# Performance work log

Hardware: AMD Instinct MI355X
Metric: run time of the kernel (lower is better)

Reference implementation:

```python
import jax, jax.numpy as jnp
import numpy as np

B, S = 8, 2048
CHANNELS, DIM, HEADS = 256, 3, 6
TCH = CHANNELS * 2  # 512
EPS = 1e-5


def _linear_init(key, out_f, in_f):
    # torch nn.Linear default init: U(-1/sqrt(in_f), 1/sqrt(in_f)) for W and b
    k1, k2 = jax.random.split(key)
    bound = 1.0 / np.sqrt(in_f)
    w = jax.random.uniform(k1, (out_f, in_f), jnp.float32, -bound, bound)
    b = jax.random.uniform(k2, (out_f,), jnp.float32, -bound, bound)
    return w, b


def setup_inputs() -> dict:
    key = jax.random.key(0)
    ks = jax.random.split(key, 8)
    x = jax.random.normal(ks[0], (B, S, TCH), jnp.float32)
    wq, bq = _linear_init(ks[1], DIM, TCH)
    wk, bk = _linear_init(ks[2], DIM, TCH)
    wv, bv = _linear_init(ks[3], DIM, TCH)
    wo, bo = _linear_init(ks[4], TCH, HEADS * DIM)
    w1, b1 = _linear_init(ks[5], TCH, TCH)
    w2, b2 = _linear_init(ks[6], TCH, TCH)
    gamma = jnp.ones((TCH,), jnp.float32)
    beta = jnp.zeros((TCH,), jnp.float32)
    return {"x": x, "wq": wq, "bq": bq, "wk": wk, "bk": bk, "wv": wv, "bv": bv,
            "wo": wo, "bo": bo, "w1": w1, "b1": b1, "w2": w2, "b2": b2,
            "gamma": gamma, "beta": beta}


def _layernorm(x, gamma, beta):
    mu = jnp.mean(x, axis=-1, keepdims=True)
    var = jnp.mean(jnp.square(x - mu), axis=-1, keepdims=True)
    return (x - mu) * jax.lax.rsqrt(var + EPS) * gamma + beta


def reference(x, wq, bq, wk, bk, wv, bv, wo, bo, w1, b1, w2, b2, gamma, beta):
    # All heads share the same w_q/w_k/w_v, so one attention pass suffices;
    # concatenating HEADS copies reproduces the original math exactly.
    q = x @ wq.T + bq                      # [B,S,DIM]
    k = x @ wk.T + bk                      # [B,S,DIM]
    v = x @ wv.T + bv                      # [B,S,DIM]
    scores = jnp.einsum('bqd,bkd->bqk', q, k) / np.sqrt(DIM)  # [B,S,S]
    soft = jax.nn.softmax(scores, axis=-1)
    z = jnp.einsum('bqk,bkd->bqd', soft, v)  # [B,S,DIM]
    z = jnp.concatenate([z] * HEADS, axis=-1)  # [B,S,HEADS*DIM]
    z = z @ wo.T + bo                       # [B,S,TCH]
    r0 = x + (z @ w1.T + b1)
    r1 = _layernorm(r0, gamma, beta)
    r1 = r1 @ w2.T + b2
    r = r0 + r1
    return _layernorm(r, gamma, beta)
```

## Files before the change

### kernel.cpp

```cpp
#include <hip/hip_runtime.h>
#include <hip/hip_bf16.h>

#define TCH 512
#define MTOT 16384
#define SEQ 2048
#define LN_EPS 1e-5f

typedef __attribute__((ext_vector_type(8))) __bf16 bf16x8;
typedef __attribute__((ext_vector_type(4))) float f32x4;

__device__ __forceinline__ unsigned pkbf(float a, float b) {
  union { __hip_bfloat16 h; unsigned short u; } ca, cb;
  ca.h = __float2bfloat16(a); cb.h = __float2bfloat16(b);
  return (unsigned)ca.u | ((unsigned)cb.u << 16);
}
__device__ __forceinline__ float bf_lo(unsigned u) { return __uint_as_float(u << 16); }
__device__ __forceinline__ float bf_hi(unsigned u) { return __uint_as_float(u & 0xffff0000u); }

__device__ __forceinline__ bf16x8 cvt8(float4 a, float4 b) {
  union { __hip_bfloat16 h; __bf16 v; } u;
  bf16x8 r;
  u.h = __float2bfloat16(a.x); r[0] = u.v;
  u.h = __float2bfloat16(a.y); r[1] = u.v;
  u.h = __float2bfloat16(a.z); r[2] = u.v;
  u.h = __float2bfloat16(a.w); r[3] = u.v;
  u.h = __float2bfloat16(b.x); r[4] = u.v;
  u.h = __float2bfloat16(b.y); r[5] = u.v;
  u.h = __float2bfloat16(b.z); r[6] = u.v;
  u.h = __float2bfloat16(b.w); r[7] = u.v;
  return r;
}

#define QSCALE 0.8329517853860118f

__global__ __launch_bounds__(256) void prep_kernel(
    const float* __restrict__ w2,
    const float* __restrict__ wo, const float* __restrict__ bo,
    const float* __restrict__ wq, const float* __restrict__ bq,
    const float* __restrict__ wk, const float* __restrict__ bk,
    const float* __restrict__ wv, const float* __restrict__ bv,
    __hip_bfloat16* __restrict__ w2b,
    float4* __restrict__ wo_eff4,
    __hip_bfloat16* __restrict__ wqkvb, float* __restrict__ qkvbias)
{
  int i = blockIdx.x * 256 + threadIdx.x;
  w2b[i] = __float2bfloat16(w2[i]);
  if (i < TCH) {
    float s0 = 0.f, s1 = 0.f, s2 = 0.f;
    #pragma unroll
    for (int h = 0; h < 6; ++h) {
      s0 += wo[i*18 + h*3 + 0];
      s1 += wo[i*18 + h*3 + 1];
      s2 += wo[i*18 + h*3 + 2];
    }
    wo_eff4[i] = make_float4(s0, s1, s2, bo[i]);
  }
  if (i < 16 * TCH) {
    int row = i >> 9, k = i & 511;
    float v;
    if      (row < 3) v = wq[row * TCH + k] * QSCALE;
    else if (row < 6) v = wk[(row - 3) * TCH + k];
    else if (row < 9) v = wv[(row - 6) * TCH + k];
    else              v = 0.f;
    wqkvb[i] = __float2bfloat16(v);
  }
  if (i < 16) {
    float v;
    if      (i < 3) v = bq[i] * QSCALE;
    else if (i < 6) v = bk[i - 3];
    else if (i < 9) v = bv[i - 6];
    else            v = 0.f;
    qkvbias[i] = v;
  }
}

__global__ __launch_bounds__(256) void prep2_kernel(
    const float* __restrict__ w1, const float* __restrict__ b1,
    const float4* __restrict__ wo_eff4, float4* __restrict__ weff4)
{
  const int t = threadIdx.x, w = t >> 6, l = t & 63;
  const int i = blockIdx.x * 4 + w;
  float sx = 0.f, sy = 0.f, sz = 0.f, sw = 0.f;
  #pragma unroll
  for (int j = 0; j < 8; ++j) {
    const int k = j * 64 + l;
    const float a = w1[(size_t)i * TCH + k];
    const float4 e = wo_eff4[k];
    sx += a * e.x; sy += a * e.y; sz += a * e.z; sw += a * e.w;
  }
  #pragma unroll
  for (int off = 1; off < 64; off <<= 1) {
    sx += __shfl_xor(sx, off, 64);
    sy += __shfl_xor(sy, off, 64);
    sz += __shfl_xor(sz, off, 64);
    sw += __shfl_xor(sw, off, 64);
  }
  if (l == 0) weff4[i] = make_float4(sx, sy, sz, sw + b1[i]);
}

__global__ __launch_bounds__(256) void qkv_kernel(
    const float* __restrict__ x,
    const __hip_bfloat16* __restrict__ wqkvb, const float* __restrict__ qkvbias,
    float4* __restrict__ q4, uint4* __restrict__ kvp)
{
  const int t = threadIdx.x, wv = t >> 6, ln = t & 63;
  const int l16 = ln & 15, quad = ln >> 4;
  const int row0 = blockIdx.x * 16;
  const int k0 = wv * 128;

  bf16x8 bfr[4];
  #pragma unroll
  for (int ks = 0; ks < 4; ++ks)
    bfr[ks] = *reinterpret_cast<const bf16x8*>(wqkvb + l16 * TCH + k0 + ks * 32 + quad * 8);

  const float* xp = x + (size_t)(row0 + l16) * TCH + k0 + quad * 8;

  f32x4 acc = {};
  #pragma unroll
  for (int ks = 0; ks < 4; ++ks) {
    float4 a = *(const float4*)(xp + ks * 32);
    float4 b = *(const float4*)(xp + ks * 32 + 4);
    acc = __builtin_amdgcn_mfma_f32_16x16x32_bf16(cvt8(a, b), bfr[ks], acc, 0, 0, 0);
  }

  __shared__ float tr[4][16][17];
  __shared__ float fin[16][17];
  #pragma unroll
  for (int r = 0; r < 4; ++r) tr[wv][quad * 4 + r][l16] = acc[r];
  __syncthreads();

  {
    const int r = t >> 4, c = t & 15;
    fin[r][c] = tr[0][r][c] + tr[1][r][c] + tr[2][r][c] + tr[3][r][c] + qkvbias[c];
  }
  __syncthreads();

  if (t < 16) {
    q4[row0 + t] = make_float4(fin[t][0], fin[t][1], fin[t][2], 0.f);
  } else if (t < 32) {
    const int r = t - 16;
    kvp[row0 + r] = make_uint4(pkbf(fin[r][3], fin[r][4]),
                               pkbf(fin[r][5], fin[r][6]),
                               pkbf(fin[r][7], fin[r][8]), 0u);
  }
}

__global__ __launch_bounds__(1024) void attn_kernel(
    const float4* __restrict__ q4, const uint4* __restrict__ kvp,
    const float* __restrict__ x, const float4* __restrict__ weff4,
    const float* __restrict__ gamma, const float* __restrict__ beta,
    __hip_bfloat16* __restrict__ r0b, __hip_bfloat16* __restrict__ r1b)
{
  __shared__ float4 part[16 * 64];
  __shared__ float4 zbuf[64];

  const int b    = blockIdx.x >> 5;
  const int qc   = blockIdx.x & 31;
  const int base = b * SEQ;
  const int tid  = threadIdx.x;
  const int wave = tid >> 6;
  const int lane = tid & 63;
  const float4 q = q4[base + qc * 64 + lane];

  const int wu = __builtin_amdgcn_readfirstlane(wave);
  const uint4* kvw = kvp + base + wu * 128;

  float l[4] = {}, a0[4] = {}, a1[4] = {}, a2[4] = {};
  #pragma unroll 4
  for (int i = 0; i < 32; ++i) {
    #pragma unroll
    for (int s = 0; s < 4; ++s) {
      uint4 rec = kvw[s * 32 + i];
      float sc = bf_lo(rec.x) * q.x + bf_hi(rec.x) * q.y + bf_lo(rec.y) * q.z;
      float p = __builtin_amdgcn_exp2f(sc);
      l[s]  += p;
      a0[s] += p * bf_hi(rec.y);
      a1[s] += p * bf_lo(rec.z);
      a2[s] += p * bf_hi(rec.z);
    }
  }
  part[wave * 64 + lane] = make_float4(l[0]+l[1]+l[2]+l[3],
                                       a0[0]+a0[1]+a0[2]+a0[3],
                                       a1[0]+a1[1]+a1[2]+a1[3],
                                       a2[0]+a2[1]+a2[2]+a2[3]);
  __syncthreads();

  if (tid < 64) {
    float L = 0.f, A0 = 0.f, A1 = 0.f, A2 = 0.f;
    #pragma unroll
    for (int w = 0; w < 16; ++w) {
      float4 p = part[w * 64 + tid];
      L += p.x; A0 += p.y; A1 += p.z; A2 += p.w;
    }
    const float inv = 1.f / L;
    zbuf[tid] = make_float4(A0 * inv, A1 * inv, A2 * inv, 0.f);
  }
  __syncthreads();

  const int c0 = lane * 8;
  float4 wv[8];
  #pragma unroll
  for (int j = 0; j < 8; ++j) wv[j] = weff4[c0 + j];
  const float4 g0  = *(const float4*)(gamma + c0);
  const float4 g1  = *(const float4*)(gamma + c0 + 4);
  const float4 be0 = *(const float4*)(beta  + c0);
  const float4 be1 = *(const float4*)(beta  + c0 + 4);
  const float gg[8] = {g0.x,g0.y,g0.z,g0.w,g1.x,g1.y,g1.z,g1.w};
  const float bb[8] = {be0.x,be0.y,be0.z,be0.w,be1.x,be1.y,be1.z,be1.w};

  #pragma unroll
  for (int qi = 0; qi < 4; ++qi) {
    const int qloc = wave * 4 + qi;
    const int grow = base + qc * 64 + qloc;
    const float4 z = zbuf[qloc];
    const float* xr = x + (size_t)grow * TCH + c0;
    const float4 x0 = *(const float4*)xr;
    const float4 x1 = *(const float4*)(xr + 4);
    const float xv[8] = {x0.x,x0.y,x0.z,x0.w,x1.x,x1.y,x1.z,x1.w};
    float r0v[8], s = 0.f, sq = 0.f;
    #pragma unroll
    for (int j = 0; j < 8; ++j) {
      float v = xv[j] + z.x * wv[j].x + z.y * wv[j].y + z.z * wv[j].z + wv[j].w;
      r0v[j] = v; s += v; sq += v * v;
    }
    #pragma unroll
    for (int off = 1; off < 64; off <<= 1) {
      s  += __shfl_xor(s,  off, 64);
      sq += __shfl_xor(sq, off, 64);
    }
    const float mu = s * (1.f / TCH);
    const float rs = rsqrtf(sq * (1.f / TCH) - mu * mu + LN_EPS);
    *(bf16x8*)(r0b + (size_t)grow * TCH + c0) =
        cvt8(make_float4(r0v[0], r0v[1], r0v[2], r0v[3]),
             make_float4(r0v[4], r0v[5], r0v[6], r0v[7]));
    float r1v[8];
    #pragma unroll
    for (int j = 0; j < 8; ++j) r1v[j] = (r0v[j] - mu) * rs * gg[j] + bb[j];
    *(bf16x8*)(r1b + (size_t)grow * TCH + c0) =
        cvt8(make_float4(r1v[0], r1v[1], r1v[2], r1v[3]),
             make_float4(r1v[4], r1v[5], r1v[6], r1v[7]));
  }
}

__global__ __launch_bounds__(256) void gemm_kernel(
    const __hip_bfloat16* __restrict__ A,
    const __hip_bfloat16* __restrict__ W,
    const float* __restrict__ bias,
    const __hip_bfloat16* __restrict__ res,
    __hip_bfloat16* __restrict__ Cout,
    float2* __restrict__ partial)
{
  __shared__ __align__(16) __hip_bfloat16 At[2][4][128][8];
  __shared__ __align__(16) __hip_bfloat16 Wt[2][4][128][8];
  __shared__ float redS[128][2];
  __shared__ float redQ[128][2];

  const int bx   = blockIdx.x;
  const int rb   = bx & 127, cb = bx >> 7;
  const int row0 = rb * 128, col0 = cb * 128;
  const int t    = threadIdx.x;
  const int w    = t >> 6, l = t & 63;
  const int l16  = l & 15, quad = l >> 4;
  const int wr   = w >> 1, wc = w & 1;
  const int srow = t & 127;
  const int sq0  = (t >> 7) << 1;

  auto stage = [&](int ks, int b) {
    #pragma unroll
    for (int j = 0; j < 2; ++j) {
      const int q = sq0 | j;
      __builtin_amdgcn_global_load_lds(
          (const __attribute__((address_space(1))) void*)(A + (size_t)(row0 + srow) * TCH + ks * 32 + q * 8),
          (__attribute__((address_space(3))) void*)&At[b][q][srow][0], 16, 0, 0);
      __builtin_amdgcn_global_load_lds(
          (const __attribute__((address_space(1))) void*)(W + (size_t)(col0 + srow) * TCH + ks * 32 + q * 8),
          (__attribute__((address_space(3))) void*)&Wt[b][q][srow][0], 16, 0, 0);
    }
  };

  f32x4 acc[4][4] = {};
  stage(0, 0);
  for (int ks = 0; ks < 16; ++ks) {
    const int cur = ks & 1;
    __syncthreads();
    if (ks < 15) stage(ks + 1, cur ^ 1);
    bf16x8 af[4], bf[4];
    #pragma unroll
    for (int mt = 0; mt < 4; ++mt)
      af[mt] = *reinterpret_cast<const bf16x8*>(&At[cur][quad][wr * 64 + mt * 16 + l16][0]);
    #pragma unroll
    for (int nt = 0; nt < 4; ++nt)
      bf[nt] = *reinterpret_cast<const bf16x8*>(&Wt[cur][quad][wc * 64 + nt * 16 + l16][0]);
    #pragma unroll
    for (int mt = 0; mt < 4; ++mt)
      #pragma unroll
      for (int nt = 0; nt < 4; ++nt)
        acc[mt][nt] = __builtin_amdgcn_mfma_f32_16x16x32_bf16(af[mt], bf[nt], acc[mt][nt], 0, 0, 0);
  }

  #pragma unroll
  for (int mt = 0; mt < 4; ++mt) {
    #pragma unroll
    for (int r = 0; r < 4; ++r) {
      const int lrow = wr * 64 + mt * 16 + quad * 4 + r;
      const int grow = row0 + lrow;
      float s = 0.f, sq = 0.f;
      #pragma unroll
      for (int nt = 0; nt < 4; ++nt) {
        const int col = col0 + wc * 64 + nt * 16 + l16;
        float v = acc[mt][nt][r] + bias[col] + __bfloat162float(res[(size_t)grow * TCH + col]);
        Cout[(size_t)grow * TCH + col] = __float2bfloat16(v);
        s += v; sq += v * v;
      }
      #pragma unroll
      for (int off = 1; off < 16; off <<= 1) {
        s  += __shfl_xor(s,  off, 64);
        sq += __shfl_xor(sq, off, 64);
      }
      if (l16 == 0) { redS[lrow][wc] = s; redQ[lrow][wc] = sq; }
    }
  }
  __syncthreads();

  if (t < 128) {
    partial[(size_t)cb * MTOT + row0 + t] =
        make_float2(redS[t][0] + redS[t][1], redQ[t][0] + redQ[t][1]);
  }
}

template<typename OUT_T>
__global__ __launch_bounds__(256) void ln_kernel(
    const __hip_bfloat16* __restrict__ Cin, const float2* __restrict__ partial,
    const float* __restrict__ gamma, const float* __restrict__ beta,
    OUT_T* __restrict__ out)
{
  const int t = threadIdx.x, wv = t >> 6, ln = t & 63;
  const int row = blockIdx.x * 4 + wv;

  float2 p0 = partial[row];
  float2 p1 = partial[MTOT + row];
  float2 p2 = partial[2 * MTOT + row];
  float2 p3 = partial[3 * MTOT + row];
  const float S = p0.x + p1.x + p2.x + p3.x;
  const float Q = p0.y + p1.y + p2.y + p3.y;
  const float mu  = S * (1.f / TCH);
  const float var = Q * (1.f / TCH) - mu * mu;
  const float rs  = rsqrtf(var + LN_EPS);

  const int c0 = ln * 8;
  bf16x8 vr = *reinterpret_cast<const bf16x8*>(Cin + (size_t)row * TCH + c0);
  float4 g0 = *(const float4*)(gamma + c0), g1 = *(const float4*)(gamma + c0 + 4);
  float4 b0 = *(const float4*)(beta  + c0), b1 = *(const float4*)(beta  + c0 + 4);

  float o[8];
  const float gg[8] = {g0.x,g0.y,g0.z,g0.w,g1.x,g1.y,g1.z,g1.w};
  const float bb[8] = {b0.x,b0.y,b0.z,b0.w,b1.x,b1.y,b1.z,b1.w};
  #pragma unroll
  for (int j = 0; j < 8; ++j) {
    union { __bf16 v; __hip_bfloat16 h; } u; u.v = vr[j];
    o[j] = (__bfloat162float(u.h) - mu) * rs * gg[j] + bb[j];
  }

  if constexpr (sizeof(OUT_T) == 2) {
    unsigned ov[4];
    #pragma unroll
    for (int j = 0; j < 4; ++j) ov[j] = pkbf(o[2*j], o[2*j+1]);
    *(uint4*)((__hip_bfloat16*)out + (size_t)row * TCH + c0) =
        make_uint4(ov[0], ov[1], ov[2], ov[3]);
  } else {
    float* op = (float*)out + (size_t)row * TCH + c0;
    *(float4*)op       = make_float4(o[0], o[1], o[2], o[3]);
    *(float4*)(op + 4) = make_float4(o[4], o[5], o[6], o[7]);
  }
}

extern "C" void kernel_launch(void* const* d_in, const int* in_sizes, int n_in,
                              void* d_out, int out_size, void* d_ws, size_t ws_size,
                              hipStream_t stream) {
  (void)in_sizes; (void)n_in; (void)out_size; (void)ws_size;
  const float* x     = (const float*)d_in[0];
  const float* wq    = (const float*)d_in[1];
  const float* bq    = (const float*)d_in[2];
  const float* wk    = (const float*)d_in[3];
  const float* bk    = (const float*)d_in[4];
  const float* wv    = (const float*)d_in[5];
  const float* bv    = (const float*)d_in[6];
  const float* wo    = (const float*)d_in[7];
  const float* bo    = (const float*)d_in[8];
  const float* w1    = (const float*)d_in[9];
  const float* b1    = (const float*)d_in[10];
  const float* w2    = (const float*)d_in[11];
  const float* b2    = (const float*)d_in[12];
  const float* gamma = (const float*)d_in[13];
  const float* beta  = (const float*)d_in[14];
  float* out = (float*)d_out;

  char* ws = (char*)d_ws;
  size_t off = 0;
  float4* q4      = (float4*)(ws + off); off += (size_t)MTOT * 16;
  uint4*  kvp     = (uint4*)(ws + off);  off += (size_t)MTOT * 16;
  float4* wo_eff4 = (float4*)(ws + off); off += (size_t)TCH * 16;
  float4* weff4   = (float4*)(ws + off); off += (size_t)TCH * 16;
  __hip_bfloat16* w2b   = (__hip_bfloat16*)(ws + off); off += (size_t)TCH * TCH * 2;
  __hip_bfloat16* wqkvb = (__hip_bfloat16*)(ws + off); off += (size_t)16 * TCH * 2;
  float*          qkvbias = (float*)(ws + off);        off += 64;
  __hip_bfloat16* r0b = (__hip_bfloat16*)(ws + off); off += (size_t)MTOT * TCH * 2;
  __hip_bfloat16* r1b = (__hip_bfloat16*)(ws + off); off += (size_t)MTOT * TCH * 2;
  __hip_bfloat16* rrb = (__hip_bfloat16*)(ws + off); off += (size_t)MTOT * TCH * 2;
  float2* part2 = (float2*)(ws + off); off += (size_t)4 * MTOT * 8;

  prep_kernel<<<(TCH*TCH)/256, 256, 0, stream>>>(
      w2, wo, bo, wq, bq, wk, bk, wv, bv, w2b, wo_eff4, wqkvb, qkvbias);
  prep2_kernel<<<TCH/4, 256, 0, stream>>>(w1, b1, wo_eff4, weff4);
  qkv_kernel<<<MTOT/16, 256, 0, stream>>>(x, wqkvb, qkvbias, q4, kvp);
  attn_kernel<<<MTOT/64, 1024, 0, stream>>>(q4, kvp, x, weff4, gamma, beta, r0b, r1b);
  gemm_kernel<<<512, 256, 0, stream>>>(r1b, w2b, b2, r0b, rrb, part2);
  ln_kernel<float><<<MTOT/4, 256, 0, stream>>>(rrb, part2, gamma, beta, out);
}
```

Before: 178.1 us.

## Split attention into score kernel and separate residual/LayerNorm epilogue kernel

```diff
diff --git a/kernel.cpp b/kernel.cpp
--- a/kernel.cpp
+++ b/kernel.cpp
@@ -145,14 +145,12 @@
   }
 }
 
-__global__ __launch_bounds__(1024) void attn_kernel(
+__global__ __launch_bounds__(1024) void attn_score_kernel(
     const float4* __restrict__ q4, const uint4* __restrict__ kvp,
-    const float* __restrict__ x, const float4* __restrict__ weff4,
-    const float* __restrict__ gamma, const float* __restrict__ beta,
-    __hip_bfloat16* __restrict__ r0b, __hip_bfloat16* __restrict__ r1b)
-{
+    float4* __restrict__ zfin)
+{
+  __shared__ uint4  kvL[2048];
   __shared__ float4 part[16 * 64];
-  __shared__ float4 zbuf[64];
 
   const int b    = blockIdx.x >> 5;
   const int qc   = blockIdx.x & 31;
@@ -160,17 +158,19 @@
   const int tid  = threadIdx.x;
   const int wave = tid >> 6;
   const int lane = tid & 63;
+
+  kvL[tid]        = kvp[base + tid];
+  kvL[tid + 1024] = kvp[base + tid + 1024];
   const float4 q = q4[base + qc * 64 + lane];
-
-  const int wu = __builtin_amdgcn_readfirstlane(wave);
-  const uint4* kvw = kvp + base + wu * 128;
-
+  __syncthreads();
+
+  const int k0 = wave * 128;
   float l[4] = {}, a0[4] = {}, a1[4] = {}, a2[4] = {};
   #pragma unroll 4
   for (int i = 0; i < 32; ++i) {
     #pragma unroll
     for (int s = 0; s < 4; ++s) {
-      uint4 rec = kvw[s * 32 + i];
+      uint4 rec = kvL[k0 + s * 32 + i];
       float sc = bf_lo(rec.x) * q.x + bf_hi(rec.x) * q.y + bf_lo(rec.y) * q.z;
       float p = __builtin_amdgcn_exp2f(sc);
       l[s]  += p;
@@ -193,14 +193,23 @@
       L += p.x; A0 += p.y; A1 += p.z; A2 += p.w;
     }
     const float inv = 1.f / L;
-    zbuf[tid] = make_float4(A0 * inv, A1 * inv, A2 * inv, 0.f);
-  }
-  __syncthreads();
+    zfin[base + qc * 64 + tid] = make_float4(A0 * inv, A1 * inv, A2 * inv, 0.f);
+  }
+}
+
+__global__ __launch_bounds__(256) void attn_epi_kernel(
+    const float4* __restrict__ zfin, const float* __restrict__ x,
+    const float4* __restrict__ weff4,
+    const float* __restrict__ gamma, const float* __restrict__ beta,
+    __hip_bfloat16* __restrict__ r0b, __hip_bfloat16* __restrict__ r1b)
+{
+  const int t = threadIdx.x, wv = t >> 6, lane = t & 63;
+  const int row0 = blockIdx.x * 16 + wv * 4;
 
   const int c0 = lane * 8;
-  float4 wv[8];
-  #pragma unroll
-  for (int j = 0; j < 8; ++j) wv[j] = weff4[c0 + j];
+  float4 wvv[8];
+  #pragma unroll
+  for (int j = 0; j < 8; ++j) wvv[j] = weff4[c0 + j];
   const float4 g0  = *(const float4*)(gamma + c0);
   const float4 g1  = *(const float4*)(gamma + c0 + 4);
   const float4 be0 = *(const float4*)(beta  + c0);
@@ -210,9 +219,8 @@
 
   #pragma unroll
   for (int qi = 0; qi < 4; ++qi) {
-    const int qloc = wave * 4 + qi;
-    const int grow = base + qc * 64 + qloc;
-    const float4 z = zbuf[qloc];
+    const int grow = row0 + qi;
+    const float4 z = zfin[grow];
     const float* xr = x + (size_t)grow * TCH + c0;
     const float4 x0 = *(const float4*)xr;
     const float4 x1 = *(const float4*)(xr + 4);
@@ -220,7 +228,7 @@
     float r0v[8], s = 0.f, sq = 0.f;
     #pragma unroll
     for (int j = 0; j < 8; ++j) {
-      float v = xv[j] + z.x * wv[j].x + z.y * wv[j].y + z.z * wv[j].z + wv[j].w;
+      float v = xv[j] + z.x * wvv[j].x + z.y * wvv[j].y + z.z * wvv[j].z + wvv[j].w;
       r0v[j] = v; s += v; sq += v * v;
     }
     #pragma unroll
@@ -399,6 +407,7 @@
   size_t off = 0;
   float4* q4      = (float4*)(ws + off); off += (size_t)MTOT * 16;
   uint4*  kvp     = (uint4*)(ws + off);  off += (size_t)MTOT * 16;
+  float4* zfin    = (float4*)(ws + off); off += (size_t)MTOT * 16;
   float4* wo_eff4 = (float4*)(ws + off); off += (size_t)TCH * 16;
   float4* weff4   = (float4*)(ws + off); off += (size_t)TCH * 16;
   __hip_bfloat16* w2b   = (__hip_bfloat16*)(ws + off); off += (size_t)TCH * TCH * 2;
@@ -413,7 +422,8 @@
       w2, wo, bo, wq, bq, wk, bk, wv, bv, w2b, wo_eff4, wqkvb, qkvbias);
   prep2_kernel<<<TCH/4, 256, 0, stream>>>(w1, b1, wo_eff4, weff4);
   qkv_kernel<<<MTOT/16, 256, 0, stream>>>(x, wqkvb, qkvbias, q4, kvp);
-  attn_kernel<<<MTOT/64, 1024, 0, stream>>>(q4, kvp, x, weff4, gamma, beta, r0b, r1b);
+  attn_score_kernel<<<MTOT/64, 1024, 0, stream>>>(q4, kvp, zfin);
+  attn_epi_kernel<<<MTOT/16, 256, 0, stream>>>(zfin, x, weff4, gamma, beta, r0b, r1b);
   gemm_kernel<<<512, 256, 0, stream>>>(r1b, w2b, b2, r0b, rrb, part2);
   ln_kernel<float><<<MTOT/4, 256, 0, stream>>>(rrb, part2, gamma, beta, out);
 }
```

New measurement: 180.4 us. Within noise of the previous version (+1.3%).

## Fuse QKV and attention into cooperative kernel; merge weight prep kernels

Applied to the files above, without the earlier changes.

```diff
diff --git a/kernel.cpp b/kernel.cpp
--- a/kernel.cpp
+++ b/kernel.cpp
@@ -1,5 +1,8 @@
 #include <hip/hip_runtime.h>
 #include <hip/hip_bf16.h>
+#include <hip/hip_cooperative_groups.h>
+
+namespace cg = cooperative_groups;
 
 #define TCH 512
 #define MTOT 16384
@@ -39,22 +42,13 @@
     const float* __restrict__ wq, const float* __restrict__ bq,
     const float* __restrict__ wk, const float* __restrict__ bk,
     const float* __restrict__ wv, const float* __restrict__ bv,
+    const float* __restrict__ w1, const float* __restrict__ b1,
     __hip_bfloat16* __restrict__ w2b,
-    float4* __restrict__ wo_eff4,
-    __hip_bfloat16* __restrict__ wqkvb, float* __restrict__ qkvbias)
+    __hip_bfloat16* __restrict__ wqkvb, float* __restrict__ qkvbias,
+    float4* __restrict__ weff4)
 {
   int i = blockIdx.x * 256 + threadIdx.x;
   w2b[i] = __float2bfloat16(w2[i]);
-  if (i < TCH) {
-    float s0 = 0.f, s1 = 0.f, s2 = 0.f;
-    #pragma unroll
-    for (int h = 0; h < 6; ++h) {
-      s0 += wo[i*18 + h*3 + 0];
-      s1 += wo[i*18 + h*3 + 1];
-      s2 += wo[i*18 + h*3 + 2];
-    }
-    wo_eff4[i] = make_float4(s0, s1, s2, bo[i]);
-  }
   if (i < 16 * TCH) {
     int row = i >> 9, k = i & 511;
     float v;
@@ -72,80 +66,80 @@
     else            v = 0.f;
     qkvbias[i] = v;
   }
-}
-
-__global__ __launch_bounds__(256) void prep2_kernel(
-    const float* __restrict__ w1, const float* __restrict__ b1,
-    const float4* __restrict__ wo_eff4, float4* __restrict__ weff4)
-{
-  const int t = threadIdx.x, w = t >> 6, l = t & 63;
-  const int i = blockIdx.x * 4 + w;
-  float sx = 0.f, sy = 0.f, sz = 0.f, sw = 0.f;
-  #pragma unroll
-  for (int j = 0; j < 8; ++j) {
-    const int k = j * 64 + l;
-    const float a = w1[(size_t)i * TCH + k];
-    const float4 e = wo_eff4[k];
-    sx += a * e.x; sy += a * e.y; sz += a * e.z; sw += a * e.w;
-  }
-  #pragma unroll
-  for (int off = 1; off < 64; off <<= 1) {
-    sx += __shfl_xor(sx, off, 64);
-    sy += __shfl_xor(sy, off, 64);
-    sz += __shfl_xor(sz, off, 64);
-    sw += __shfl_xor(sw, off, 64);
-  }
-  if (l == 0) weff4[i] = make_float4(sx, sy, sz, sw + b1[i]);
-}
-
-__global__ __launch_bounds__(256) void qkv_kernel(
+  if (blockIdx.x < 128) {
+    const int t = threadIdx.x, w = t >> 6, l = t & 63;
+    const int row = blockIdx.x * 4 + w;
+    float sx = 0.f, sy = 0.f, sz = 0.f, sw = 0.f;
+    #pragma unroll
+    for (int j = 0; j < 8; ++j) {
+      const int k = j * 64 + l;
+      float e0 = 0.f, e1 = 0.f, e2 = 0.f;
+      #pragma unroll
+      for (int h = 0; h < 6; ++h) {
+        e0 += wo[k*18 + h*3 + 0];
+        e1 += wo[k*18 + h*3 + 1];
+        e2 += wo[k*18 + h*3 + 2];
+      }
+      const float a = w1[(size_t)row * TCH + k];
+      sx += a * e0; sy += a * e1; sz += a * e2; sw += a * bo[k];
+    }
+    #pragma unroll
+    for (int off = 1; off < 64; off <<= 1) {
+      sx += __shfl_xor(sx, off, 64);
+      sy += __shfl_xor(sy, off, 64);
+      sz += __shfl_xor(sz, off, 64);
+      sw += __shfl_xor(sw, off, 64);
+    }
+    if (l == 0) weff4[row] = make_float4(sx, sy, sz, sw + b1[row]);
+  }
+}
+
+__device__ __forceinline__ void qkv_phase(
     const float* __restrict__ x,
     const __hip_bfloat16* __restrict__ wqkvb, const float* __restrict__ qkvbias,
     float4* __restrict__ q4, uint4* __restrict__ kvp)
 {
-  const int t = threadIdx.x, wv = t >> 6, ln = t & 63;
-  const int l16 = ln & 15, quad = ln >> 4;
-  const int row0 = blockIdx.x * 16;
-  const int k0 = wv * 128;
+  __shared__ float tr[4][4][16][17];
+
+  const int tid  = threadIdx.x;
+  const int wave = tid >> 6, lane = tid & 63;
+  const int l16  = lane & 15, quad = lane >> 4;
+  const int ks4  = wave >> 2, rg = wave & 3;
+  const int grow0 = blockIdx.x * 64;
+  const int r0 = grow0 + rg * 16;
+  const int k0 = ks4 * 128;
 
   bf16x8 bfr[4];
   #pragma unroll
-  for (int ks = 0; ks < 4; ++ks)
-    bfr[ks] = *reinterpret_cast<const bf16x8*>(wqkvb + l16 * TCH + k0 + ks * 32 + quad * 8);
-
-  const float* xp = x + (size_t)(row0 + l16) * TCH + k0 + quad * 8;
-
+  for (int ksj = 0; ksj < 4; ++ksj)
+    bfr[ksj] = *reinterpret_cast<const bf16x8*>(wqkvb + l16 * TCH + k0 + ksj * 32 + quad * 8);
+
+  const float* xp = x + (size_t)(r0 + l16) * TCH + k0 + quad * 8;
   f32x4 acc = {};
   #pragma unroll
-  for (int ks = 0; ks < 4; ++ks) {
-    float4 a = *(const float4*)(xp + ks * 32);
-    float4 b = *(const float4*)(xp + ks * 32 + 4);
-    acc = __builtin_amdgcn_mfma_f32_16x16x32_bf16(cvt8(a, b), bfr[ks], acc, 0, 0, 0);
-  }
-
-  __shared__ float tr[4][16][17];
-  __shared__ float fin[16][17];
-  #pragma unroll
-  for (int r = 0; r < 4; ++r) tr[wv][quad * 4 + r][l16] = acc[r];
+  for (int ksj = 0; ksj < 4; ++ksj) {
+    float4 a = *(const float4*)(xp + ksj * 32);
+    float4 b = *(const float4*)(xp + ksj * 32 + 4);
+    acc = __builtin_amdgcn_mfma_f32_16x16x32_bf16(cvt8(a, b), bfr[ksj], acc, 0, 0, 0);
+  }
+  #pragma unroll
+  for (int r = 0; r < 4; ++r) tr[ks4][rg][quad * 4 + r][l16] = acc[r];
   __syncthreads();
 
-  {
-    const int r = t >> 4, c = t & 15;
-    fin[r][c] = tr[0][r][c] + tr[1][r][c] + tr[2][r][c] + tr[3][r][c] + qkvbias[c];
-  }
-  __syncthreads();
-
-  if (t < 16) {
-    q4[row0 + t] = make_float4(fin[t][0], fin[t][1], fin[t][2], 0.f);
-  } else if (t < 32) {
-    const int r = t - 16;
-    kvp[row0 + r] = make_uint4(pkbf(fin[r][3], fin[r][4]),
-                               pkbf(fin[r][5], fin[r][6]),
-                               pkbf(fin[r][7], fin[r][8]), 0u);
-  }
-}
-
-__global__ __launch_bounds__(1024) void attn_kernel(
+  if (tid < 64) {
+    const int row = tid, rgg = row >> 4, rr = row & 15;
+    float c[9];
+    #pragma unroll
+    for (int j = 0; j < 9; ++j)
+      c[j] = tr[0][rgg][rr][j] + tr[1][rgg][rr][j] + tr[2][rgg][rr][j]
+           + tr[3][rgg][rr][j] + qkvbias[j];
+    q4[grow0 + row] = make_float4(c[0], c[1], c[2], 0.f);
+    kvp[grow0 + row] = make_uint4(pkbf(c[3], c[4]), pkbf(c[5], c[6]),
+                                  pkbf(c[7], c[8]), 0u);
+  }
+}
+
+__device__ __forceinline__ void attn_phase(
     const float4* __restrict__ q4, const uint4* __restrict__ kvp,
     const float* __restrict__ x, const float4* __restrict__ weff4,
     const float* __restrict__ gamma, const float* __restrict__ beta,
@@ -154,8 +148,9 @@
   __shared__ float4 part[16 * 64];
   __shared__ float4 zbuf[64];
 
-  const int b    = blockIdx.x >> 5;
-  const int qc   = blockIdx.x & 31;
+  const int bi   = blockIdx.x;
+  const int b    = bi >> 5;
+  const int qc   = bi & 31;
   const int base = b * SEQ;
   const int tid  = threadIdx.x;
   const int wave = tid >> 6;
@@ -198,9 +193,9 @@
   __syncthreads();
 
   const int c0 = lane * 8;
-  float4 wv[8];
-  #pragma unroll
-  for (int j = 0; j < 8; ++j) wv[j] = weff4[c0 + j];
+  float4 wvv[8];
+  #pragma unroll
+  for (int j = 0; j < 8; ++j) wvv[j] = weff4[c0 + j];
   const float4 g0  = *(const float4*)(gamma + c0);
   const float4 g1  = *(const float4*)(gamma + c0 + 4);
   const float4 be0 = *(const float4*)(beta  + c0);
@@ -220,7 +215,7 @@
     float r0v[8], s = 0.f, sq = 0.f;
     #pragma unroll
     for (int j = 0; j < 8; ++j) {
-      float v = xv[j] + z.x * wv[j].x + z.y * wv[j].y + z.z * wv[j].z + wv[j].w;
+      float v = xv[j] + z.x * wvv[j].x + z.y * wvv[j].y + z.z * wvv[j].z + wvv[j].w;
       r0v[j] = v; s += v; sq += v * v;
     }
     #pragma unroll
@@ -240,6 +235,36 @@
         cvt8(make_float4(r1v[0], r1v[1], r1v[2], r1v[3]),
              make_float4(r1v[4], r1v[5], r1v[6], r1v[7]));
   }
+}
+
+__global__ __launch_bounds__(1024) void qkvattn_coop(
+    const float* __restrict__ x, const __hip_bfloat16* __restrict__ wqkvb,
+    const float* __restrict__ qkvbias, float4* __restrict__ q4,
+    uint4* __restrict__ kvp, const float4* __restrict__ weff4,
+    const float* __restrict__ gamma, const float* __restrict__ beta,
+    __hip_bfloat16* __restrict__ r0b, __hip_bfloat16* __restrict__ r1b)
+{
+  qkv_phase(x, wqkvb, qkvbias, q4, kvp);
+  __threadfence();
+  cg::this_grid().sync();
+  attn_phase(q4, kvp, x, weff4, gamma, beta, r0b, r1b);
+}
+
+__global__ __launch_bounds__(1024) void qkv_solo(
+    const float* __restrict__ x, const __hip_bfloat16* __restrict__ wqkvb,
+    const float* __restrict__ qkvbias, float4* __restrict__ q4,
+    uint4* __restrict__ kvp)
+{
+  qkv_phase(x, wqkvb, qkvbias, q4, kvp);
+}
+
+__global__ __launch_bounds__(1024) void attn_solo(
+    const float4* __restrict__ q4, const uint4* __restrict__ kvp,
+    const float* __restrict__ x, const float4* __restrict__ weff4,
+    const float* __restrict__ gamma, const float* __restrict__ beta,
+    __hip_bfloat16* __restrict__ r0b, __hip_bfloat16* __restrict__ r1b)
+{
+  attn_phase(q4, kvp, x, weff4, gamma, beta, r0b, r1b);
 }
 
 __global__ __launch_bounds__(256) void gemm_kernel(
@@ -399,7 +424,6 @@
   size_t off = 0;
   float4* q4      = (float4*)(ws + off); off += (size_t)MTOT * 16;
   uint4*  kvp     = (uint4*)(ws + off);  off += (size_t)MTOT * 16;
-  float4* wo_eff4 = (float4*)(ws + off); off += (size_t)TCH * 16;
   float4* weff4   = (float4*)(ws + off); off += (size_t)TCH * 16;
   __hip_bfloat16* w2b   = (__hip_bfloat16*)(ws + off); off += (size_t)TCH * TCH * 2;
   __hip_bfloat16* wqkvb = (__hip_bfloat16*)(ws + off); off += (size_t)16 * TCH * 2;
@@ -410,10 +434,22 @@
   float2* part2 = (float2*)(ws + off); off += (size_t)4 * MTOT * 8;
 
   prep_kernel<<<(TCH*TCH)/256, 256, 0, stream>>>(
-      w2, wo, bo, wq, bq, wk, bk, wv, bv, w2b, wo_eff4, wqkvb, qkvbias);
-  prep2_kernel<<<TCH/4, 256, 0, stream>>>(w1, b1, wo_eff4, weff4);
-  qkv_kernel<<<MTOT/16, 256, 0, stream>>>(x, wqkvb, qkvbias, q4, kvp);
-  attn_kernel<<<MTOT/64, 1024, 0, stream>>>(q4, kvp, x, weff4, gamma, beta, r0b, r1b);
+      w2, wo, bo, wq, bq, wk, bk, wv, bv, w1, b1, w2b, wqkvb, qkvbias, weff4);
+
+  {
+    void* kargs[] = {
+      (void*)&x, (void*)&wqkvb, (void*)&qkvbias, (void*)&q4, (void*)&kvp,
+      (void*)&weff4, (void*)&gamma, (void*)&beta, (void*)&r0b, (void*)&r1b
+    };
+    hipError_t ce = hipLaunchCooperativeKernel(
+        reinterpret_cast<const void*>(&qkvattn_coop),
+        dim3(MTOT / 64), dim3(1024), kargs, 0u, stream);
+    if (ce != hipSuccess) {
+      qkv_solo<<<MTOT / 64, 1024, 0, stream>>>(x, wqkvb, qkvbias, q4, kvp);
+      attn_solo<<<MTOT / 64, 1024, 0, stream>>>(q4, kvp, x, weff4, gamma, beta, r0b, r1b);
+    }
+  }
+
   gemm_kernel<<<512, 256, 0, stream>>>(r1b, w2b, b2, r0b, rrb, part2);
   ln_kernel<float><<<MTOT/4, 256, 0, stream>>>(rrb, part2, gamma, beta, out);
 }
```

Result: slower. 286.3 us (+60.7%).

## Fold prep2 into prep kernel and halve attention block size

Applied to the files above, without the earlier changes.

```diff
diff --git a/kernel.cpp b/kernel.cpp
--- a/kernel.cpp
+++ b/kernel.cpp
@@ -39,22 +39,13 @@
     const float* __restrict__ wq, const float* __restrict__ bq,
     const float* __restrict__ wk, const float* __restrict__ bk,
     const float* __restrict__ wv, const float* __restrict__ bv,
+    const float* __restrict__ w1, const float* __restrict__ b1,
     __hip_bfloat16* __restrict__ w2b,
-    float4* __restrict__ wo_eff4,
-    __hip_bfloat16* __restrict__ wqkvb, float* __restrict__ qkvbias)
+    __hip_bfloat16* __restrict__ wqkvb, float* __restrict__ qkvbias,
+    float4* __restrict__ weff4)
 {
   int i = blockIdx.x * 256 + threadIdx.x;
   w2b[i] = __float2bfloat16(w2[i]);
-  if (i < TCH) {
-    float s0 = 0.f, s1 = 0.f, s2 = 0.f;
-    #pragma unroll
-    for (int h = 0; h < 6; ++h) {
-      s0 += wo[i*18 + h*3 + 0];
-      s1 += wo[i*18 + h*3 + 1];
-      s2 += wo[i*18 + h*3 + 2];
-    }
-    wo_eff4[i] = make_float4(s0, s1, s2, bo[i]);
-  }
   if (i < 16 * TCH) {
     int row = i >> 9, k = i & 511;
     float v;
@@ -72,30 +63,32 @@
     else            v = 0.f;
     qkvbias[i] = v;
   }
-}
-
-__global__ __launch_bounds__(256) void prep2_kernel(
-    const float* __restrict__ w1, const float* __restrict__ b1,
-    const float4* __restrict__ wo_eff4, float4* __restrict__ weff4)
-{
-  const int t = threadIdx.x, w = t >> 6, l = t & 63;
-  const int i = blockIdx.x * 4 + w;
-  float sx = 0.f, sy = 0.f, sz = 0.f, sw = 0.f;
-  #pragma unroll
-  for (int j = 0; j < 8; ++j) {
-    const int k = j * 64 + l;
-    const float a = w1[(size_t)i * TCH + k];
-    const float4 e = wo_eff4[k];
-    sx += a * e.x; sy += a * e.y; sz += a * e.z; sw += a * e.w;
-  }
-  #pragma unroll
-  for (int off = 1; off < 64; off <<= 1) {
-    sx += __shfl_xor(sx, off, 64);
-    sy += __shfl_xor(sy, off, 64);
-    sz += __shfl_xor(sz, off, 64);
-    sw += __shfl_xor(sw, off, 64);
-  }
-  if (l == 0) weff4[i] = make_float4(sx, sy, sz, sw + b1[i]);
+  if (blockIdx.x < 128) {
+    const int t = threadIdx.x, w = t >> 6, l = t & 63;
+    const int row = blockIdx.x * 4 + w;
+    float sx = 0.f, sy = 0.f, sz = 0.f, sw = 0.f;
+    #pragma unroll
+    for (int j = 0; j < 8; ++j) {
+      const int k = j * 64 + l;
+      float e0 = 0.f, e1 = 0.f, e2 = 0.f;
+      #pragma unroll
+      for (int h = 0; h < 6; ++h) {
+        e0 += wo[k*18 + h*3 + 0];
+        e1 += wo[k*18 + h*3 + 1];
+        e2 += wo[k*18 + h*3 + 2];
+      }
+      const float a = w1[(size_t)row * TCH + k];
+      sx += a * e0; sy += a * e1; sz += a * e2; sw += a * bo[k];
+    }
+    #pragma unroll
+    for (int off = 1; off < 64; off <<= 1) {
+      sx += __shfl_xor(sx, off, 64);
+      sy += __shfl_xor(sy, off, 64);
+      sz += __shfl_xor(sz, off, 64);
+      sw += __shfl_xor(sw, off, 64);
+    }
+    if (l == 0) weff4[row] = make_float4(sx, sy, sz, sw + b1[row]);
+  }
 }
 
 __global__ __launch_bounds__(256) void qkv_kernel(
@@ -145,13 +138,13 @@
   }
 }
 
-__global__ __launch_bounds__(1024) void attn_kernel(
+__global__ __launch_bounds__(512) void attn_kernel(
     const float4* __restrict__ q4, const uint4* __restrict__ kvp,
     const float* __restrict__ x, const float4* __restrict__ weff4,
     const float* __restrict__ gamma, const float* __restrict__ beta,
     __hip_bfloat16* __restrict__ r0b, __hip_bfloat16* __restrict__ r1b)
 {
-  __shared__ float4 part[16 * 64];
+  __shared__ float4 part[8 * 64];
   __shared__ float4 zbuf[64];
 
   const int b    = blockIdx.x >> 5;
@@ -163,14 +156,14 @@
   const float4 q = q4[base + qc * 64 + lane];
 
   const int wu = __builtin_amdgcn_readfirstlane(wave);
-  const uint4* kvw = kvp + base + wu * 128;
+  const uint4* kvw = kvp + base + wu * 256;
 
   float l[4] = {}, a0[4] = {}, a1[4] = {}, a2[4] = {};
-  #pragma unroll 4
-  for (int i = 0; i < 32; ++i) {
+  #pragma unroll 2
+  for (int i = 0; i < 64; ++i) {
     #pragma unroll
     for (int s = 0; s < 4; ++s) {
-      uint4 rec = kvw[s * 32 + i];
+      uint4 rec = kvw[s * 64 + i];
       float sc = bf_lo(rec.x) * q.x + bf_hi(rec.x) * q.y + bf_lo(rec.y) * q.z;
       float p = __builtin_amdgcn_exp2f(sc);
       l[s]  += p;
@@ -188,7 +181,7 @@
   if (tid < 64) {
     float L = 0.f, A0 = 0.f, A1 = 0.f, A2 = 0.f;
     #pragma unroll
-    for (int w = 0; w < 16; ++w) {
+    for (int w = 0; w < 8; ++w) {
       float4 p = part[w * 64 + tid];
       L += p.x; A0 += p.y; A1 += p.z; A2 += p.w;
     }
@@ -198,9 +191,9 @@
   __syncthreads();
 
   const int c0 = lane * 8;
-  float4 wv[8];
-  #pragma unroll
-  for (int j = 0; j < 8; ++j) wv[j] = weff4[c0 + j];
+  float4 wvv[8];
+  #pragma unroll
+  for (int j = 0; j < 8; ++j) wvv[j] = weff4[c0 + j];
   const float4 g0  = *(const float4*)(gamma + c0);
   const float4 g1  = *(const float4*)(gamma + c0 + 4);
   const float4 be0 = *(const float4*)(beta  + c0);
@@ -209,8 +202,8 @@
   const float bb[8] = {be0.x,be0.y,be0.z,be0.w,be1.x,be1.y,be1.z,be1.w};
 
   #pragma unroll
-  for (int qi = 0; qi < 4; ++qi) {
-    const int qloc = wave * 4 + qi;
+  for (int qi = 0; qi < 8; ++qi) {
+    const int qloc = wave * 8 + qi;
     const int grow = base + qc * 64 + qloc;
     const float4 z = zbuf[qloc];
     const float* xr = x + (size_t)grow * TCH + c0;
@@ -220,7 +213,7 @@
     float r0v[8], s = 0.f, sq = 0.f;
     #pragma unroll
     for (int j = 0; j < 8; ++j) {
-      float v = xv[j] + z.x * wv[j].x + z.y * wv[j].y + z.z * wv[j].z + wv[j].w;
+      float v = xv[j] + z.x * wvv[j].x + z.y * wvv[j].y + z.z * wvv[j].z + wvv[j].w;
       r0v[j] = v; s += v; sq += v * v;
     }
     #pragma unroll
@@ -399,7 +392,6 @@
   size_t off = 0;
   float4* q4      = (float4*)(ws + off); off += (size_t)MTOT * 16;
   uint4*  kvp     = (uint4*)(ws + off);  off += (size_t)MTOT * 16;
-  float4* wo_eff4 = (float4*)(ws + off); off += (size_t)TCH * 16;
   float4* weff4   = (float4*)(ws + off); off += (size_t)TCH * 16;
   __hip_bfloat16* w2b   = (__hip_bfloat16*)(ws + off); off += (size_t)TCH * TCH * 2;
   __hip_bfloat16* wqkvb = (__hip_bfloat16*)(ws + off); off += (size_t)16 * TCH * 2;
@@ -410,10 +402,9 @@
   float2* part2 = (float2*)(ws + off); off += (size_t)4 * MTOT * 8;
 
   prep_kernel<<<(TCH*TCH)/256, 256, 0, stream>>>(
-      w2, wo, bo, wq, bq, wk, bk, wv, bv, w2b, wo_eff4, wqkvb, qkvbias);
-  prep2_kernel<<<TCH/4, 256, 0, stream>>>(w1, b1, wo_eff4, weff4);
+      w2, wo, bo, wq, bq, wk, bk, wv, bv, w1, b1, w2b, wqkvb, qkvbias, weff4);
   qkv_kernel<<<MTOT/16, 256, 0, stream>>>(x, wqkvb, qkvbias, q4, kvp);
-  attn_kernel<<<MTOT/64, 1024, 0, stream>>>(q4, kvp, x, weff4, gamma, beta, r0b, r1b);
+  attn_kernel<<<MTOT/64, 512, 0, stream>>>(q4, kvp, x, weff4, gamma, beta, r0b, r1b);
   gemm_kernel<<<512, 256, 0, stream>>>(r1b, w2b, b2, r0b, rrb, part2);
   ln_kernel<float><<<MTOT/4, 256, 0, stream>>>(rrb, part2, gamma, beta, out);
 }
```

New measurement: 180.9 us. No clear change (+1.5%).
